# Performance work log

Measured on AMD Instinct MI355X. Metric: run time of the kernel, lower is better.

## Reference

```python
import jax, jax.numpy as jnp
import numpy as np


def setup_inputs() -> dict:
    key = jax.random.key(0)
    k1, k2 = jax.random.split(key)
    B, C_in, C_out, H, W = 16, 64, 64, 256, 256
    MH, MW = 8, 12
    x = jax.random.normal(k1, (B, C_in, H, W), dtype=jnp.float32)
    scale = 1.0 / np.sqrt(C_in * C_out).astype(np.float32)
    weight = scale * jax.random.normal(k2, (C_in, C_out, MH, MW, 2), dtype=jnp.float32)
    return {"x": x, "weight": weight}


def reference(x, weight):
    B, C, H, W = x.shape
    Wr = W // 2 + 1  # rfft width
    mh = min(weight.shape[2], H)
    mw = min(weight.shape[3], Wr)
    # FFT to frequency domain (orthonormal), keep only low-frequency block
    x_ft = jnp.fft.rfft2(x, norm='ortho')  # (B, C_in, H, Wr) complex
    w_cplx = (weight[..., 0] + 1j * weight[..., 1])[:, :, :mh, :mw]  # (C_in, C_out, mh, mw)
    out_modes = jnp.einsum('bixy,ioxy->boxy', x_ft[:, :, :mh, :mw], w_cplx)
    out_ft = jnp.zeros((B, weight.shape[1], H, Wr), dtype=out_modes.dtype)
    out_ft = out_ft.at[:, :, :mh, :mw].set(out_modes)
    return jnp.fft.irfft2(out_ft, s=(H, W), norm='ortho')
```

## Files before the change

kernel.cpp:

```cpp
#include <hip/hip_runtime.h>
#include <math.h>

#define PI2 6.2831853071795864769f


__global__ __launch_bounds__(256) void k1_fwd(const float* __restrict__ x,
                                              float* __restrict__ Xm) {
  __shared__ float tw[128][16];
  __shared__ float lds[2][4096];
  const int img  = blockIdx.x;
  const int wv   = threadIdx.x >> 6;
  const int lane = threadIdx.x & 63;

  {
    int h = threadIdx.x >> 1;
    int kyb = (threadIdx.x & 1) * 4;
#pragma unroll
    for (int j = 0; j < 4; ++j) {
      int ky = kyb + j;
      float th = PI2 * (float)((ky * h) & 255) * (1.0f / 256.0f);
      float s_, c_;
      __sincosf(th, &s_, &c_);
      tw[h][ky * 2] = c_;
      tw[h][ky * 2 + 1] = -s_;
    }
  }
  __syncthreads();

  float aR[8][4], aI[8][4];
#pragma unroll
  for (int ky = 0; ky < 8; ++ky)
#pragma unroll
    for (int j = 0; j < 4; ++j) { aR[ky][j] = 0.0f; aI[ky][j] = 0.0f; }

  const float* xa = x + (size_t)img * 65536 + (size_t)(wv * 32) * 256 + lane * 4;
  const float* xb = xa + 128 * 256;
  for (int it = 0; it < 32; ++it) {
    const int h = wv * 32 + it;
    float4 va = *(const float4*)xa;
    float4 vb = *(const float4*)xb;
    xa += 256; xb += 256;
    float p0 = va.x + vb.x, p1 = va.y + vb.y, p2 = va.z + vb.z, p3 = va.w + vb.w;
    float m0 = va.x - vb.x, m1 = va.y - vb.y, m2 = va.z - vb.z, m3 = va.w - vb.w;
#pragma unroll
    for (int ky = 0; ky < 8; ++ky) {
      float c  = tw[h][ky * 2];
      float ns = tw[h][ky * 2 + 1];
      float u0, u1, u2, u3;
      if (ky & 1) { u0 = m0; u1 = m1; u2 = m2; u3 = m3; }
      else        { u0 = p0; u1 = p1; u2 = p2; u3 = p3; }
      aR[ky][0] = fmaf(u0, c, aR[ky][0]);  aI[ky][0] = fmaf(u0, ns, aI[ky][0]);
      aR[ky][1] = fmaf(u1, c, aR[ky][1]);  aI[ky][1] = fmaf(u1, ns, aI[ky][1]);
      aR[ky][2] = fmaf(u2, c, aR[ky][2]);  aI[ky][2] = fmaf(u2, ns, aI[ky][2]);
      aR[ky][3] = fmaf(u3, c, aR[ky][3]);  aI[ky][3] = fmaf(u3, ns, aI[ky][3]);
    }
  }

  if (wv < 2) {
#pragma unroll
    for (int ky = 0; ky < 8; ++ky)
#pragma unroll
      for (int j = 0; j < 4; ++j) {
        int p = (ky * 256 + lane * 4 + j) * 2;
        lds[wv][p] = aR[ky][j];
        lds[wv][p + 1] = aI[ky][j];
      }
  }
  __syncthreads();
  if (wv >= 2) {
#pragma unroll
    for (int ky = 0; ky < 8; ++ky)
#pragma unroll
      for (int j = 0; j < 4; ++j) {
        int p = (ky * 256 + lane * 4 + j) * 2;
        lds[wv - 2][p] += aR[ky][j];
        lds[wv - 2][p + 1] += aI[ky][j];
      }
  }
  __syncthreads();
  for (int f = threadIdx.x; f < 4096; f += 256) lds[0][f] += lds[1][f];
  __syncthreads();

  if (threadIdx.x < 96) {
    int ky = threadIdx.x / 12, kx = threadIdx.x % 12;
    float Cw, Sw;
    __sincosf(PI2 * (float)kx * (1.0f / 256.0f), &Sw, &Cw);
    float c = 1.0f, s = 0.0f, Xr = 0.0f, Xi = 0.0f;
    const float* base = &lds[0][ky * 512];
    for (int w = 0; w < 256; ++w) {
      float Sre = base[w * 2], Sim = base[w * 2 + 1];
      Xr += Sre * c + Sim * s;
      Xi += Sim * c - Sre * s;
      float nc = fmaf(c, Cw, -s * Sw);
      s = fmaf(s, Cw, c * Sw);
      c = nc;
    }
    float2 v = { Xr * (1.0f / 256.0f), Xi * (1.0f / 256.0f) };
    ((float2*)Xm)[(size_t)threadIdx.x * 1024 + img] = v;
  }
}

__global__ __launch_bounds__(256) void k3_mix(const float* __restrict__ Xm,
                                              const float* __restrict__ wt,
                                              float* __restrict__ Fm) {
  __shared__ float Xs[1024 * 2];
  __shared__ float Ws[4096 * 2];
  const int pos = blockIdx.x;
  for (int idx = threadIdx.x; idx < 2048; idx += 256)
    Xs[idx] = Xm[(size_t)pos * 2048 + idx];
  for (int idx = threadIdx.x; idx < 4096; idx += 256) {
    Ws[idx * 2]     = wt[((size_t)idx * 96 + pos) * 2];
    Ws[idx * 2 + 1] = wt[((size_t)idx * 96 + pos) * 2 + 1];
  }
  __syncthreads();
  const int b = threadIdx.x >> 4;
  const int og = (threadIdx.x & 15) * 4;
  float ar[4] = {0, 0, 0, 0}, ai[4] = {0, 0, 0, 0};
  for (int i = 0; i < 64; ++i) {
    float xr = Xs[(b * 64 + i) * 2], xi = Xs[(b * 64 + i) * 2 + 1];
#pragma unroll
    for (int r = 0; r < 4; ++r) {
      float wr = Ws[(i * 64 + og + r) * 2], wi = Ws[(i * 64 + og + r) * 2 + 1];
      ar[r] += xr * wr - xi * wi;
      ai[r] += xr * wi + xi * wr;
    }
  }
#pragma unroll
  for (int r = 0; r < 4; ++r) {
    Fm[((size_t)(b * 64 + og + r) * 96 + pos) * 2]     = ar[r];
    Fm[((size_t)(b * 64 + og + r) * 96 + pos) * 2 + 1] = ai[r];
  }
}

__global__ __launch_bounds__(256) void k4a_invh(const float* __restrict__ Fm,
                                                float* __restrict__ U) {
  __shared__ float Fs[192];
  const int img2 = blockIdx.x;
  if (threadIdx.x < 192) Fs[threadIdx.x] = Fm[(size_t)img2 * 192 + threadIdx.x];
  __syncthreads();
  const int h = threadIdx.x;
  float cc[8], ss[8];
#pragma unroll
  for (int ky = 0; ky < 8; ++ky) {
    float th = PI2 * (float)((ky * h) & 255) * (1.0f / 256.0f);
    __sincosf(th, &ss[ky], &cc[ky]);
  }
  float4 ov4[6];
  float* ov = (float*)ov4;
#pragma unroll
  for (int kx = 0; kx < 12; ++kx) {
    float Ur = 0.0f, Ui = 0.0f;
#pragma unroll
    for (int ky = 0; ky < 8; ++ky) {
      float Fr = Fs[(ky * 12 + kx) * 2], Fi = Fs[(ky * 12 + kx) * 2 + 1];
      Ur += Fr * cc[ky] - Fi * ss[ky];
      Ui += Fr * ss[ky] + Fi * cc[ky];
    }
    float a = (kx == 0 ? 1.0f : 2.0f) * (1.0f / 256.0f);
    ov[kx * 2] = Ur * a;
    ov[kx * 2 + 1] = Ui * a;
  }
  float4* dst = (float4*)(U + ((size_t)img2 * 256 + h) * 24);
#pragma unroll
  for (int k = 0; k < 6; ++k) dst[k] = ov4[k];
}

__global__ __launch_bounds__(256) void k4b_invw(const float* __restrict__ U,
                                                float* __restrict__ outp) {
  const int img2 = blockIdx.x;
  const int w = threadIdx.x;
  float c[12], ns[12];
#pragma unroll
  for (int kx = 0; kx < 12; ++kx) {
    float th = PI2 * (float)((kx * w) & 255) * (1.0f / 256.0f);
    float s_;
    __sincosf(th, &s_, &c[kx]);
    ns[kx] = -s_;
  }
  const float* ub = U + (size_t)img2 * 6144;
  float* ob = outp + (size_t)img2 * 65536 + w;
  for (int h = 0; h < 256; ++h) {
    float4 u4[6];
    const float4* us = (const float4*)(ub + h * 24);
#pragma unroll
    for (int k = 0; k < 6; ++k) u4[k] = us[k];
    const float* u = (const float*)u4;
    float acc = 0.0f;
#pragma unroll
    for (int kx = 0; kx < 12; ++kx)
      acc = fmaf(u[kx * 2], c[kx], fmaf(u[kx * 2 + 1], ns[kx], acc));
    ob[h * 256] = acc;
  }
}

extern "C" void kernel_launch(void* const* d_in, const int* in_sizes, int n_in,
                              void* d_out, int out_size, void* d_ws, size_t ws_size,
                              hipStream_t stream) {
  const float* x  = (const float*)d_in[0];
  const float* wt = (const float*)d_in[1];
  float* outp = (float*)d_out;

  float* Xm = (float*)d_ws;
  float* Fm = Xm + 196608;
  float* U  = Fm + 196608;

  k1_fwd  <<<1024, 256, 0, stream>>>(x, Xm);
  k3_mix  <<<  96, 256, 0, stream>>>(Xm, wt, Fm);
  k4a_invh<<<1024, 256, 0, stream>>>(Fm, U);
  k4b_invw<<<1024, 256, 0, stream>>>(U, outp);
}
```

Before: 531.7 us.

## Fuse mode mixing and inverse FFT stages into one kernel per output image

```diff
diff --git a/kernel.cpp b/kernel.cpp
--- a/kernel.cpp
+++ b/kernel.cpp
@@ -96,100 +96,118 @@
       c = nc;
     }
     float2 v = { Xr * (1.0f / 256.0f), Xi * (1.0f / 256.0f) };
-    ((float2*)Xm)[(size_t)threadIdx.x * 1024 + img] = v;
+    const int bb = img >> 6, ii = img & 63;
+    ((float2*)Xm)[(size_t)(bb * 96 + threadIdx.x) * 64 + ii] = v;
   }
 }
 
-__global__ __launch_bounds__(256) void k3_mix(const float* __restrict__ Xm,
-                                              const float* __restrict__ wt,
-                                              float* __restrict__ Fm) {
-  __shared__ float Xs[1024 * 2];
-  __shared__ float Ws[4096 * 2];
-  const int pos = blockIdx.x;
-  for (int idx = threadIdx.x; idx < 2048; idx += 256)
-    Xs[idx] = Xm[(size_t)pos * 2048 + idx];
-  for (int idx = threadIdx.x; idx < 4096; idx += 256) {
-    Ws[idx * 2]     = wt[((size_t)idx * 96 + pos) * 2];
-    Ws[idx * 2 + 1] = wt[((size_t)idx * 96 + pos) * 2 + 1];
-  }
-  __syncthreads();
-  const int b = threadIdx.x >> 4;
-  const int og = (threadIdx.x & 15) * 4;
-  float ar[4] = {0, 0, 0, 0}, ai[4] = {0, 0, 0, 0};
-  for (int i = 0; i < 64; ++i) {
-    float xr = Xs[(b * 64 + i) * 2], xi = Xs[(b * 64 + i) * 2 + 1];
-#pragma unroll
-    for (int r = 0; r < 4; ++r) {
-      float wr = Ws[(i * 64 + og + r) * 2], wi = Ws[(i * 64 + og + r) * 2 + 1];
-      ar[r] += xr * wr - xi * wi;
-      ai[r] += xr * wi + xi * wr;
-    }
-  }
-#pragma unroll
-  for (int r = 0; r < 4; ++r) {
-    Fm[((size_t)(b * 64 + og + r) * 96 + pos) * 2]     = ar[r];
-    Fm[((size_t)(b * 64 + og + r) * 96 + pos) * 2 + 1] = ai[r];
-  }
-}
-
-__global__ __launch_bounds__(256) void k4a_invh(const float* __restrict__ Fm,
-                                                float* __restrict__ U) {
+__global__ __launch_bounds__(256) void k2_fused(const float* __restrict__ Xm,
+                                                const float* __restrict__ wt,
+                                                float* __restrict__ outp) {
+  __shared__ float sh[6528];
   __shared__ float Fs[192];
   const int img2 = blockIdx.x;
-  if (threadIdx.x < 192) Fs[threadIdx.x] = Fm[(size_t)img2 * 192 + threadIdx.x];
-  __syncthreads();
-  const int h = threadIdx.x;
-  float cc[8], ss[8];
-#pragma unroll
-  for (int ky = 0; ky < 8; ++ky) {
-    float th = PI2 * (float)((ky * h) & 255) * (1.0f / 256.0f);
-    __sincosf(th, &ss[ky], &cc[ky]);
-  }
-  float4 ov4[6];
-  float* ov = (float*)ov4;
-#pragma unroll
-  for (int kx = 0; kx < 12; ++kx) {
-    float Ur = 0.0f, Ui = 0.0f;
+  const int b = img2 >> 6, o = img2 & 63;
+  const int tid = threadIdx.x;
+
+  float fr = 0.0f, fi = 0.0f;
+#pragma unroll
+  for (int c = 0; c < 2; ++c) {
+    for (int idx = tid; idx < 1536; idx += 256) {
+      int p = idx >> 4, j4 = idx & 15;
+      float4 v = ((const float4*)(Xm + (size_t)(b * 96 + p) * 128 + c * 64))[j4];
+      ((float4*)(sh + p * 68))[j4] = v;
+    }
+    __syncthreads();
+    if (tid < 96) {
+      const int pos = tid;
+      const float* wrow = wt + ((size_t)(c * 2048 + o) * 96 + pos) * 2;
+#pragma unroll 8
+      for (int jj = 0; jj < 32; ++jj) {
+        float xr = sh[pos * 68 + 2 * jj];
+        float xi = sh[pos * 68 + 2 * jj + 1];
+        float wr = wrow[(size_t)jj * 12288];
+        float wi = wrow[(size_t)jj * 12288 + 1];
+        fr += xr * wr - xi * wi;
+        fi += xr * wi + xi * wr;
+      }
+    }
+    __syncthreads();
+  }
+  if (tid < 96) { Fs[tid * 2] = fr; Fs[tid * 2 + 1] = fi; }
+  __syncthreads();
+
+  {
+    const int h = tid;
+    float cc[8], ss[8];
 #pragma unroll
     for (int ky = 0; ky < 8; ++ky) {
-      float Fr = Fs[(ky * 12 + kx) * 2], Fi = Fs[(ky * 12 + kx) * 2 + 1];
-      Ur += Fr * cc[ky] - Fi * ss[ky];
-      Ui += Fr * ss[ky] + Fi * cc[ky];
-    }
-    float a = (kx == 0 ? 1.0f : 2.0f) * (1.0f / 256.0f);
-    ov[kx * 2] = Ur * a;
-    ov[kx * 2 + 1] = Ui * a;
-  }
-  float4* dst = (float4*)(U + ((size_t)img2 * 256 + h) * 24);
-#pragma unroll
-  for (int k = 0; k < 6; ++k) dst[k] = ov4[k];
-}
-
-__global__ __launch_bounds__(256) void k4b_invw(const float* __restrict__ U,
-                                                float* __restrict__ outp) {
-  const int img2 = blockIdx.x;
-  const int w = threadIdx.x;
-  float c[12], ns[12];
-#pragma unroll
-  for (int kx = 0; kx < 12; ++kx) {
-    float th = PI2 * (float)((kx * w) & 255) * (1.0f / 256.0f);
-    float s_;
-    __sincosf(th, &s_, &c[kx]);
-    ns[kx] = -s_;
-  }
-  const float* ub = U + (size_t)img2 * 6144;
-  float* ob = outp + (size_t)img2 * 65536 + w;
-  for (int h = 0; h < 256; ++h) {
-    float4 u4[6];
-    const float4* us = (const float4*)(ub + h * 24);
-#pragma unroll
-    for (int k = 0; k < 6; ++k) u4[k] = us[k];
-    const float* u = (const float*)u4;
-    float acc = 0.0f;
-#pragma unroll
-    for (int kx = 0; kx < 12; ++kx)
-      acc = fmaf(u[kx * 2], c[kx], fmaf(u[kx * 2 + 1], ns[kx], acc));
-    ob[h * 256] = acc;
+      float th = PI2 * (float)((ky * h) & 255) * (1.0f / 256.0f);
+      __sincosf(th, &ss[ky], &cc[ky]);
+    }
+    float4 ov4[6];
+    float* ov = (float*)ov4;
+#pragma unroll
+    for (int kx = 0; kx < 12; ++kx) {
+      float Ur = 0.0f, Ui = 0.0f;
+#pragma unroll
+      for (int ky = 0; ky < 8; ++ky) {
+        float Fr = Fs[(ky * 12 + kx) * 2], Fi = Fs[(ky * 12 + kx) * 2 + 1];
+        Ur += Fr * cc[ky] - Fi * ss[ky];
+        Ui += Fr * ss[ky] + Fi * cc[ky];
+      }
+      float a = (kx == 0 ? 1.0f : 2.0f) * (1.0f / 256.0f);
+      ov[kx * 2] = Ur * a;
+      ov[kx * 2 + 1] = Ui * a;
+    }
+    float4* dst = (float4*)(sh + h * 24);
+#pragma unroll
+    for (int k = 0; k < 6; ++k) dst[k] = ov4[k];
+  }
+  __syncthreads();
+
+  {
+    const int wv = tid >> 6, lane = tid & 63;
+    float cx[12], sx[12];
+#pragma unroll
+    for (int kx = 0; kx < 12; ++kx) {
+      float th = PI2 * (float)((kx * lane) & 255) * (1.0f / 256.0f);
+      __sincosf(th, &sx[kx], &cx[kx]);
+    }
+    float* ob = outp + (size_t)img2 * 65536 + lane;
+    for (int l0 = 0; l0 < 64; ++l0) {
+      const int h = wv * 64 + l0;
+      const float4* ur = (const float4*)(sh + h * 24);
+      float u[24];
+#pragma unroll
+      for (int k = 0; k < 6; ++k) {
+        float4 q = ur[k];
+        u[4 * k] = q.x; u[4 * k + 1] = q.y; u[4 * k + 2] = q.z; u[4 * k + 3] = q.w;
+      }
+      float A[4] = {0.0f, 0.0f, 0.0f, 0.0f};
+      float B1 = 0.0f, B3 = 0.0f;
+#pragma unroll
+      for (int kx = 0; kx < 12; ++kx) {
+        const int cls = kx & 3;
+        A[cls] = fmaf(u[2 * kx], cx[kx], A[cls]);
+        A[cls] = fmaf(-u[2 * kx + 1], sx[kx], A[cls]);
+        if (cls == 1) {
+          B1 = fmaf(u[2 * kx], sx[kx], B1);
+          B1 = fmaf(u[2 * kx + 1], cx[kx], B1);
+        }
+        if (cls == 3) {
+          B3 = fmaf(u[2 * kx], sx[kx], B3);
+          B3 = fmaf(u[2 * kx + 1], cx[kx], B3);
+        }
+      }
+      float t0 = A[0] + A[2], t1 = A[1] + A[3];
+      float t2 = A[0] - A[2], t3 = B3 - B1;
+      float* row = ob + h * 256;
+      row[0]   = t0 + t1;
+      row[64]  = t2 + t3;
+      row[128] = t0 - t1;
+      row[192] = t2 - t3;
+    }
   }
 }
 
@@ -201,11 +219,7 @@
   float* outp = (float*)d_out;
 
   float* Xm = (float*)d_ws;
-  float* Fm = Xm + 196608;
-  float* U  = Fm + 196608;
 
   k1_fwd  <<<1024, 256, 0, stream>>>(x, Xm);
-  k3_mix  <<<  96, 256, 0, stream>>>(Xm, wt, Fm);
-  k4a_invh<<<1024, 256, 0, stream>>>(Fm, U);
-  k4b_invw<<<1024, 256, 0, stream>>>(U, outp);
+  k2_fused<<<1024, 256, 0, stream>>>(Xm, wt, outp);
 }
```

Result: faster. 477.4 us (-10.2%).
